# Kernel optimization log

Measured on AMD Instinct MI355X. Metric: run time of the kernel, lower is better.

Reference implementation:

```python
import jax, jax.numpy as jnp
import numpy as np

EPS_REG = 0.05      # epsilon (entropic regularization), learn_epsilon=False
NUM_ITERS = 20      # Sinkhorn iterations
MESH_ITERS = 3      # MESH sharpening iterations


def setup_inputs() -> dict:
    key = jax.random.key(0)
    k1, k2, k3, k4 = jax.random.split(key, 4)
    B, K, M, D = 2048, 64, 64, 256
    slots_q = jax.random.normal(k1, (B, K, D), dtype=jnp.float32)
    slots_r = jax.random.normal(k2, (B, M, D), dtype=jnp.float32)
    mask_q = jnp.ones((B, K), dtype=jnp.float32)
    mask_r = jnp.ones((B, M), dtype=jnp.float32)
    W1 = jax.random.normal(k3, (D, D), dtype=jnp.float32) * (1.0 / np.sqrt(D))
    b1 = jnp.zeros((D,), dtype=jnp.float32)
    W2 = jax.random.normal(k4, (D, D), dtype=jnp.float32) * (1.0 / np.sqrt(D))
    b2 = jnp.zeros((D,), dtype=jnp.float32)
    return {"slots_q": slots_q, "slots_r": slots_r, "mask_q": mask_q,
            "mask_r": mask_r, "W1": W1, "b1": b1, "W2": W2, "b2": b2}


def _cost_proj(x, W1, b1, W2, b2):
    h = jax.nn.relu(jnp.einsum('bnd,de->bne', x, W1) + b1)
    return jnp.einsum('bnd,de->bne', h, W2) + b2


def _cdist(q, r):
    # Euclidean pairwise distance: [B,K,M]
    q2 = jnp.sum(q * q, axis=-1)                      # [B,K]
    r2 = jnp.sum(r * r, axis=-1)                      # [B,M]
    qr = jnp.einsum('bkd,bmd->bkm', q, r)             # [B,K,M]
    d2 = q2[:, :, None] + r2[:, None, :] - 2.0 * qr
    return jnp.sqrt(jnp.clip(d2, 0.0))


def _sinkhorn(C, mask_q, mask_r):
    log_K = -C / EPS_REG
    log_K = log_K + jnp.log(jnp.clip(mask_q, 1e-8))[:, :, None]
    log_K = log_K + jnp.log(jnp.clip(mask_r, 1e-8))[:, None, :]
    B, K, M = C.shape
    la0 = jnp.zeros((B, K, 1), dtype=C.dtype)
    lb0 = jnp.zeros((B, 1, M), dtype=C.dtype)

    def body(i, carry):
        la, lb = carry
        la = -jax.nn.logsumexp(log_K + lb, axis=2, keepdims=True)
        lb = -jax.nn.logsumexp(log_K + la, axis=1, keepdims=True)
        return (la, lb)

    la, lb = jax.lax.fori_loop(0, NUM_ITERS, body, (la0, lb0))
    return jnp.exp(log_K + la + lb)


def _mesh(T):
    def body(i, T):
        Ts = T * T
        Ts = Ts / (jnp.sum(Ts, axis=-1, keepdims=True) + 1e-8)
        Ts = Ts / (jnp.sum(Ts, axis=-2, keepdims=True) + 1e-8)
        return Ts
    return jax.lax.fori_loop(0, MESH_ITERS, body, T)


def reference(slots_q, slots_r, mask_q, mask_r, W1, b1, W2, b2):
    q_proj = _cost_proj(slots_q, W1, b1, W2, b2)
    r_proj = _cost_proj(slots_r, W1, b1, W2, b2)
    C = _cdist(q_proj, r_proj)                        # [B,K,M]
    T = _sinkhorn(C, mask_q, mask_r)                  # [B,K,M]
    T_hard = _mesh(T)
    transport_cost = jnp.sum(T_hard * C, axis=(-1, -2))   # [B]
    similarity = jax.nn.sigmoid(-transport_cost)           # [B]
    return similarity, T_hard, C, transport_cost
```

## Files before the change

### kernel.cpp

```cpp
#include <hip/hip_runtime.h>


typedef __attribute__((ext_vector_type(8))) short s16x8;
typedef __attribute__((ext_vector_type(4))) float f32x4;

#define OFF_T  2048
#define OFF_C  (2048 + 2048 * 4096)
#define OFF_TC (2048 + 2 * 2048 * 4096)

__device__ __forceinline__ unsigned short f2bf(float x) {
  unsigned u = __builtin_bit_cast(unsigned, x);
  u += 0x7fffu + ((u >> 16) & 1u);
  return (unsigned short)(u >> 16);
}
__device__ __forceinline__ unsigned cvtpk(float lo, float hi) {
  unsigned r;
  asm("v_cvt_pk_bf16_f32 %0, %1, %2" : "=v"(r) : "v"(lo), "v"(hi));
  return r;
}

#define MFMA16(a, b, c) __builtin_amdgcn_mfma_f32_16x16x32_bf16((a), (b), (c), 0, 0, 0)

__global__ void __launch_bounds__(256)
prep_w_kernel(const float* __restrict__ W1, const float* __restrict__ W2,
              short* __restrict__ W1p, short* __restrict__ W2p) {
  int i = blockIdx.x * 256 + threadIdx.x;
  int k = i >> 8, col = i & 255;
  int p = (col >> 4) * 4096 + (k >> 5) * 512 +
          (((k >> 3) & 3) * 16 + (col & 15)) * 8 + (k & 7);
  W1p[p] = (short)f2bf(W1[i]);
  W2p[p] = (short)f2bf(W2[i]);
}

__device__ __forceinline__ void gemm_kloop(const short* __restrict__ wb,
                                           const char* sm, int abase0, int asw,
                                           int koff0, f32x4 (&acc)[4][8]) {
  s16x8 bw[4][4];
#pragma unroll
  for (int p = 0; p < 4; ++p)
#pragma unroll
    for (int nf = 0; nf < 4; ++nf)
      bw[p][nf] = *(const s16x8*)(wb + nf * 4096 + p * 512);
#pragma unroll
  for (int ks = 0; ks < 8; ++ks) {
    const int ko = (ks * 64 + koff0) ^ asw;
    s16x8 af[8];
#pragma unroll
    for (int rf = 0; rf < 8; ++rf)
      af[rf] = *(const s16x8*)(sm + rf * 8192 + abase0 + ko);
#pragma unroll
    for (int rf = 0; rf < 8; ++rf)
#pragma unroll
      for (int nf = 0; nf < 4; ++nf)
        acc[nf][rf] = MFMA16(bw[ks & 3][nf], af[rf], acc[nf][rf]);
    if (ks < 4) {
#pragma unroll
      for (int nf = 0; nf < 4; ++nf)
        bw[ks & 3][nf] = *(const s16x8*)(wb + nf * 4096 + (ks + 4) * 512);
    }
  }
}

__global__ void __launch_bounds__(256, 2)
proj_cost_kernel(const float* __restrict__ slots_q, const float* __restrict__ slots_r,
                 const short* __restrict__ W1p, const short* __restrict__ W2p,
                 const float* __restrict__ b1, const float* __restrict__ b2,
                 float* __restrict__ out) {
  __shared__ char smem[65536];
  float* nbuf = (float*)smem;

  const int b    = blockIdx.x;
  const int tid  = threadIdx.x;
  const int wv   = tid >> 6;
  const int lane = tid & 63;
  const int l15  = lane & 15;
  const int lhi  = lane >> 4;

  {
    const float* sq = slots_q + (size_t)b * 16384;
    const float* sr = slots_r + (size_t)b * 16384;
#pragma unroll
    for (int half = 0; half < 2; ++half) {
      float4 tmp[16];
#pragma unroll
      for (int i = 0; i < 16; ++i) {
        int idx4 = tid + 256 * (half * 16 + i);
        tmp[i] = (half == 0) ? *(const float4*)(sq + idx4 * 4)
                             : *(const float4*)(sr + (idx4 - 4096) * 4);
      }
#pragma unroll
      for (int i = 0; i < 16; ++i) {
        int idx4 = tid + 256 * (half * 16 + i);
        int row = idx4 >> 6;
        int colb = (idx4 & 63) * 8;
        *(uint2*)(smem + row * 512 + (colb ^ ((row & 7) << 4))) =
            make_uint2(cvtpk(tmp[i].x, tmp[i].y), cvtpk(tmp[i].z, tmp[i].w));
      }
    }
  }
  __syncthreads();

  const int abase0 = l15 * 512;
  const int asw    = (l15 & 7) << 4;
  const int koff0  = lhi * 16;
  const short* wb1 = W1p + wv * 4 * 4096 + lane * 8;
  const short* wb2 = W2p + wv * 4 * 4096 + lane * 8;

  float4 b1v[4], b2v[4];
#pragma unroll
  for (int ef = 0; ef < 4; ++ef) {
    b1v[ef] = *(const float4*)(b1 + wv * 64 + ef * 16 + lhi * 4);
    b2v[ef] = *(const float4*)(b2 + wv * 64 + ef * 16 + lhi * 4);
  }

  const f32x4 z4 = {0.f, 0.f, 0.f, 0.f};
  f32x4 acc[4][8];

#pragma unroll
  for (int ef = 0; ef < 4; ++ef)
#pragma unroll
    for (int rf = 0; rf < 8; ++rf) acc[ef][rf] = z4;
  gemm_kloop(wb1, smem, abase0, asw, koff0, acc);
  __syncthreads();
#pragma unroll
  for (int ef = 0; ef < 4; ++ef) {
    const int eb = (wv * 64 + ef * 16 + lhi * 4) * 2;
#pragma unroll
    for (int rf = 0; rf < 8; ++rf) {
      float a0 = fmaxf(acc[ef][rf][0] + b1v[ef].x, 0.0f);
      float a1 = fmaxf(acc[ef][rf][1] + b1v[ef].y, 0.0f);
      float a2 = fmaxf(acc[ef][rf][2] + b1v[ef].z, 0.0f);
      float a3 = fmaxf(acc[ef][rf][3] + b1v[ef].w, 0.0f);
      *(uint2*)(smem + rf * 8192 + abase0 + (eb ^ asw)) =
          make_uint2(cvtpk(a0, a1), cvtpk(a2, a3));
    }
  }
  __syncthreads();

#pragma unroll
  for (int ef = 0; ef < 4; ++ef)
#pragma unroll
    for (int rf = 0; rf < 8; ++rf) acc[ef][rf] = z4;
  gemm_kloop(wb2, smem, abase0, asw, koff0, acc);
  __syncthreads();

  float pn[8] = {0.f, 0.f, 0.f, 0.f, 0.f, 0.f, 0.f, 0.f};
#pragma unroll
  for (int ef = 0; ef < 4; ++ef) {
    const int eb = (wv * 64 + ef * 16 + lhi * 4) * 2;
#pragma unroll
    for (int rf = 0; rf < 8; ++rf) {
      float a0 = acc[ef][rf][0] + b2v[ef].x;
      float a1 = acc[ef][rf][1] + b2v[ef].y;
      float a2 = acc[ef][rf][2] + b2v[ef].z;
      float a3 = acc[ef][rf][3] + b2v[ef].w;
      pn[rf] += a0 * a0 + a1 * a1 + a2 * a2 + a3 * a3;
      *(uint2*)(smem + rf * 8192 + abase0 + (eb ^ asw)) =
          make_uint2(cvtpk(a0, a1), cvtpk(a2, a3));
    }
  }
#pragma unroll
  for (int rf = 0; rf < 8; ++rf) {
    pn[rf] += __shfl_xor(pn[rf], 16);
    pn[rf] += __shfl_xor(pn[rf], 32);
  }
  __syncthreads();

  f32x4 accC[4];
#pragma unroll
  for (int n = 0; n < 4; ++n) accC[n] = z4;
#pragma unroll
  for (int ks = 0; ks < 8; ++ks) {
    const int ko = (ks * 64 + koff0) ^ asw;
    s16x8 aQ = *(const s16x8*)(smem + wv * 8192 + abase0 + ko);
#pragma unroll
    for (int n = 0; n < 4; ++n) {
      s16x8 bR = *(const s16x8*)(smem + 32768 + n * 8192 + abase0 + ko);
      accC[n] = MFMA16(aQ, bR, accC[n]);
    }
  }
  __syncthreads();

  if (lhi == 0) {
#pragma unroll
    for (int rf = 0; rf < 8; ++rf) nbuf[wv * 128 + rf * 16 + l15] = pn[rf];
  }
  __syncthreads();

  f32x4 nq = z4;
#pragma unroll
  for (int w = 0; w < 4; ++w)
    nq += *(const f32x4*)(nbuf + w * 128 + wv * 16 + lhi * 4);
  float nR[4];
#pragma unroll
  for (int n = 0; n < 4; ++n) {
    float s = 0.0f;
#pragma unroll
    for (int w = 0; w < 4; ++w) s += nbuf[w * 128 + 64 + n * 16 + l15];
    nR[n] = s;
  }

  float* Cb = out + OFF_C + (size_t)b * 4096;
#pragma unroll
  for (int n = 0; n < 4; ++n)
#pragma unroll
    for (int j = 0; j < 4; ++j) {
      float d2 = nq[j] + nR[n] - 2.0f * accC[n][j];
      Cb[(wv * 16 + lhi * 4 + j) * 64 + n * 16 + l15] = sqrtf(fmaxf(d2, 0.0f));
    }
}

__global__ void __launch_bounds__(256, 8)
sinkhorn_solve(const float* __restrict__ mask_r, float* __restrict__ out) {
  __shared__ float tile[64 * 65];
  __shared__ float u_arr[64], w_arr[64], red[4];

  const int b    = blockIdx.x;
  const int tid  = threadIdx.x;
  const int wv   = tid >> 6;
  const int lane = tid & 63;
  const int rk   = tid >> 2;
  const int g    = tid & 3;
  const int e0   = g * 16;

  const float* Cb = out + OFF_C + (size_t)b * 4096;

#pragma unroll
  for (int i = 0; i < 16; ++i) {
    int idx = tid + 256 * i;
    tile[(idx >> 6) * 65 + (idx & 63)] = Cb[idx];
  }
  if (tid < 64) w_arr[tid] = __logf(fmaxf(mask_r[(size_t)b * 64 + tid], 1e-8f));
  __syncthreads();

  float cn[16];
#pragma unroll
  for (int i = 0; i < 16; ++i) cn[i] = tile[rk * 65 + e0 + i] * -20.0f;

  for (int it = 0; it < 20; ++it) {
    {
      float v[16];
#pragma unroll
      for (int i = 0; i < 16; ++i) v[i] = cn[i] + w_arr[e0 + i];
      float mx = v[0];
#pragma unroll
      for (int i = 1; i < 16; ++i) mx = fmaxf(mx, v[i]);
      float s = 0.0f;
#pragma unroll
      for (int i = 0; i < 16; ++i) s += __expf(v[i] - mx);
#pragma unroll
      for (int d = 1; d < 4; d <<= 1) {
        float mo = __shfl_xor(mx, d), so = __shfl_xor(s, d);
        float nm = fmaxf(mx, mo);
        s = s * __expf(mx - nm) + so * __expf(mo - nm);
        mx = nm;
      }
      if (g == 0) u_arr[rk] = -(mx + __logf(s));
    }
    __syncthreads();
    {
      float v[16];
#pragma unroll
      for (int i = 0; i < 16; ++i)
        v[i] = tile[(e0 + i) * 65 + rk] * -20.0f + u_arr[e0 + i];
      float mx = v[0];
#pragma unroll
      for (int i = 1; i < 16; ++i) mx = fmaxf(mx, v[i]);
      float s = 0.0f;
#pragma unroll
      for (int i = 0; i < 16; ++i) s += __expf(v[i] - mx);
#pragma unroll
      for (int d = 1; d < 4; d <<= 1) {
        float mo = __shfl_xor(mx, d), so = __shfl_xor(s, d);
        float nm = fmaxf(mx, mo);
        s = s * __expf(mx - nm) + so * __expf(mo - nm);
        mx = nm;
      }
      if (g == 0) w_arr[rk] = -(mx + __logf(s));
    }
    __syncthreads();
  }

  float t[16];
  {
    float uk = u_arr[rk];
#pragma unroll
    for (int i = 0; i < 16; ++i) t[i] = __expf(cn[i] + uk + w_arr[e0 + i]);
  }
  for (int it = 0; it < 3; ++it) {
    if (it > 0) {
      __syncthreads();
#pragma unroll
      for (int i = 0; i < 16; ++i) t[i] = tile[rk * 65 + e0 + i];
    }
    float s = 0.0f;
#pragma unroll
    for (int i = 0; i < 16; ++i) { t[i] *= t[i]; s += t[i]; }
    s += __shfl_xor(s, 1); s += __shfl_xor(s, 2);
    float inv = 1.0f / (s + 1e-8f);
#pragma unroll
    for (int i = 0; i < 16; ++i) tile[rk * 65 + e0 + i] = t[i] * inv;
    __syncthreads();
    float tc[16]; float cs = 0.0f;
#pragma unroll
    for (int i = 0; i < 16; ++i) { tc[i] = tile[(e0 + i) * 65 + rk]; cs += tc[i]; }
    cs += __shfl_xor(cs, 1); cs += __shfl_xor(cs, 2);
    inv = 1.0f / (cs + 1e-8f);
#pragma unroll
    for (int i = 0; i < 16; ++i) tile[(e0 + i) * 65 + rk] = tc[i] * inv;
  }
  __syncthreads();

  {
    float part = 0.0f;
#pragma unroll
    for (int i = 0; i < 16; ++i)
      part += tile[rk * 65 + e0 + i] * (cn[i] * -0.05f);
#pragma unroll
    for (int d = 1; d < 64; d <<= 1) part += __shfl_xor(part, d);
    if (lane == 0) red[wv] = part;
  }
  __syncthreads();
  if (tid == 0) {
    float tc = red[0] + red[1] + red[2] + red[3];
    out[OFF_TC + b] = tc;
    out[b] = 1.0f / (1.0f + __expf(tc));
  }
  {
    float* Tout = out + OFF_T + (size_t)b * 4096;
#pragma unroll
    for (int i = 0; i < 16; ++i) {
      int idx = tid + 256 * i;
      Tout[idx] = tile[(idx >> 6) * 65 + (idx & 63)];
    }
  }
}

extern "C" void kernel_launch(void* const* d_in, const int* in_sizes, int n_in,
                              void* d_out, int out_size, void* d_ws, size_t ws_size,
                              hipStream_t stream) {
  const float* slots_q = (const float*)d_in[0];
  const float* slots_r = (const float*)d_in[1];
  const float* mask_r = (const float*)d_in[3];
  const float* W1 = (const float*)d_in[4];
  const float* b1 = (const float*)d_in[5];
  const float* W2 = (const float*)d_in[6];
  const float* b2 = (const float*)d_in[7];

  short* W1p = (short*)d_ws;
  short* W2p = W1p + 65536;

  prep_w_kernel<<<256, 256, 0, stream>>>(W1, W2, W1p, W2p);
  proj_cost_kernel<<<2048, 256, 0, stream>>>(slots_q, slots_r, W1p, W2p, b1, b2,
                                             (float*)d_out);
  sinkhorn_solve<<<2048, 256, 0, stream>>>(mask_r, (float*)d_out);
}
```

Before: 249.0 us.

## Fuse projection/cost kernel with Sinkhorn solve and keep C in shared memory

```diff
diff --git a/kernel.cpp b/kernel.cpp
--- a/kernel.cpp
+++ b/kernel.cpp
@@ -62,12 +62,16 @@
 }
 
 __global__ void __launch_bounds__(256, 2)
-proj_cost_kernel(const float* __restrict__ slots_q, const float* __restrict__ slots_r,
-                 const short* __restrict__ W1p, const short* __restrict__ W2p,
-                 const float* __restrict__ b1, const float* __restrict__ b2,
-                 float* __restrict__ out) {
+sinkhorn_fused(const float* __restrict__ slots_q, const float* __restrict__ slots_r,
+               const short* __restrict__ W1p, const short* __restrict__ W2p,
+               const float* __restrict__ b1, const float* __restrict__ b2,
+               const float* __restrict__ mask_r, float* __restrict__ out) {
   __shared__ char smem[65536];
-  float* nbuf = (float*)smem;
+  float* nbuf  = (float*)smem;
+  float* tile  = (float*)smem;
+  float* u_arr = (float*)(smem + 16640);
+  float* w_arr = u_arr + 64;
+  float* red   = w_arr + 64;
 
   const int b    = blockIdx.x;
   const int tid  = threadIdx.x;
@@ -75,6 +79,9 @@
   const int lane = tid & 63;
   const int l15  = lane & 15;
   const int lhi  = lane >> 4;
+
+  float mr = 1.0f;
+  if (tid < 64) mr = mask_r[(size_t)b * 64 + tid];
 
   {
     const float* sq = slots_q + (size_t)b * 16384;
@@ -199,43 +206,39 @@
     for (int w = 0; w < 4; ++w) s += nbuf[w * 128 + 64 + n * 16 + l15];
     nR[n] = s;
   }
-
-  float* Cb = out + OFF_C + (size_t)b * 4096;
+  __syncthreads();
+
 #pragma unroll
   for (int n = 0; n < 4; ++n)
 #pragma unroll
     for (int j = 0; j < 4; ++j) {
+      int k = wv * 16 + lhi * 4 + j;
+      int m = n * 16 + l15;
       float d2 = nq[j] + nR[n] - 2.0f * accC[n][j];
-      Cb[(wv * 16 + lhi * 4 + j) * 64 + n * 16 + l15] = sqrtf(fmaxf(d2, 0.0f));
-    }
-}
-
-__global__ void __launch_bounds__(256, 8)
-sinkhorn_solve(const float* __restrict__ mask_r, float* __restrict__ out) {
-  __shared__ float tile[64 * 65];
-  __shared__ float u_arr[64], w_arr[64], red[4];
-
-  const int b    = blockIdx.x;
-  const int tid  = threadIdx.x;
-  const int wv   = tid >> 6;
-  const int lane = tid & 63;
-  const int rk   = tid >> 2;
-  const int g    = tid & 3;
-  const int e0   = g * 16;
-
-  const float* Cb = out + OFF_C + (size_t)b * 4096;
-
+      tile[k * 65 + m] = sqrtf(fmaxf(d2, 0.0f));
+    }
+  if (tid < 64) w_arr[tid] = __logf(fmaxf(mr, 1e-8f));
+  __syncthreads();
+
+  {
+    float* Cb = out + OFF_C + (size_t)b * 4096;
+#pragma unroll
+    for (int i = 0; i < 16; ++i) {
+      int idx = tid + 256 * i;
+      Cb[idx] = tile[(idx >> 6) * 65 + (idx & 63)];
+    }
+  }
+
+  const int rk = tid >> 2;
+  const int g  = tid & 3;
+  const int e0 = g * 16;
+
+  float cn[16], cc[16];
 #pragma unroll
   for (int i = 0; i < 16; ++i) {
-    int idx = tid + 256 * i;
-    tile[(idx >> 6) * 65 + (idx & 63)] = Cb[idx];
-  }
-  if (tid < 64) w_arr[tid] = __logf(fmaxf(mask_r[(size_t)b * 64 + tid], 1e-8f));
-  __syncthreads();
-
-  float cn[16];
-#pragma unroll
-  for (int i = 0; i < 16; ++i) cn[i] = tile[rk * 65 + e0 + i] * -20.0f;
+    cn[i] = tile[rk * 65 + e0 + i] * -20.0f;
+    cc[i] = tile[(e0 + i) * 65 + rk] * -20.0f;
+  }
 
   for (int it = 0; it < 20; ++it) {
     {
@@ -261,8 +264,7 @@
     {
       float v[16];
 #pragma unroll
-      for (int i = 0; i < 16; ++i)
-        v[i] = tile[(e0 + i) * 65 + rk] * -20.0f + u_arr[e0 + i];
+      for (int i = 0; i < 16; ++i) v[i] = cc[i] + u_arr[e0 + i];
       float mx = v[0];
 #pragma unroll
       for (int i = 1; i < 16; ++i) mx = fmaxf(mx, v[i]);
@@ -322,9 +324,9 @@
   }
   __syncthreads();
   if (tid == 0) {
-    float tc = red[0] + red[1] + red[2] + red[3];
-    out[OFF_TC + b] = tc;
-    out[b] = 1.0f / (1.0f + __expf(tc));
+    float tcv = red[0] + red[1] + red[2] + red[3];
+    out[OFF_TC + b] = tcv;
+    out[b] = 1.0f / (1.0f + __expf(tcv));
   }
   {
     float* Tout = out + OFF_T + (size_t)b * 4096;
@@ -351,7 +353,6 @@
   short* W2p = W1p + 65536;
 
   prep_w_kernel<<<256, 256, 0, stream>>>(W1, W2, W1p, W2p);
-  proj_cost_kernel<<<2048, 256, 0, stream>>>(slots_q, slots_r, W1p, W2p, b1, b2,
-                                             (float*)d_out);
-  sinkhorn_solve<<<2048, 256, 0, stream>>>(mask_r, (float*)d_out);
-}
+  sinkhorn_fused<<<2048, 256, 0, stream>>>(slots_q, slots_r, W1p, W2p, b1, b2,
+                                           mask_r, (float*)d_out);
+}
```

Result: no change. 251.7 us (+1.1%).
